# Kernel optimization log

Measured on AMD Instinct MI355X. Metric: run time of the kernel, lower is better.

The kernel has to match this reference:

```python
import jax, jax.numpy as jnp
import numpy as np
from jax import lax

B, IN_C, DIM, HEADS, K = 8, 64, 128, 4, 3
H, W = 96, 96
HEAD_DIM = DIM // HEADS
SCALE = HEAD_DIM ** -0.5
EPS = 1e-5  # BatchNorm eps (eval mode, running_mean=0, running_var=1)


def _conv3x3(x, w):
    return lax.conv_general_dilated(x, w, (1, 1), ((1, 1), (1, 1)),
                                    dimension_numbers=('NCHW', 'OIHW', 'NCHW'))


def _cbr(x, w, g, b):
    y = _conv3x3(x, w)
    y = y * (g / jnp.sqrt(1.0 + EPS))[None, :, None, None] + b[None, :, None, None]
    return jax.nn.relu(y)


def setup_inputs() -> dict:
    key = jax.random.key(0)
    ks = jax.random.split(key, 24)
    n = lambda i, s, sc=0.05: jax.random.normal(ks[i], s, jnp.float32) * sc
    u = lambda i, s: jax.random.uniform(ks[i], s, jnp.float32, 0.5, 1.5)
    return dict(
        x=jax.random.normal(ks[0], (B, IN_C, H, W), jnp.float32),
        fg=jax.random.normal(ks[1], (B, DIM, H, W), jnp.float32),
        conv1_w=n(2, (DIM, IN_C, 3, 3)), bn1_g=u(3, (DIM,)), bn1_b=n(4, (DIM,)),
        conv2_w=n(5, (DIM, DIM, 3, 3)), bn2_g=u(6, (DIM,)), bn2_b=n(7, (DIM,)),
        v_w=n(8, (DIM, DIM)), v_b=n(9, (DIM,)),
        attn_w=n(10, (K ** 4 * HEADS, DIM)), attn_b=n(11, (K ** 4 * HEADS,)),
        proj_w=n(12, (DIM, DIM)), proj_b=n(13, (DIM,)),
        conv3_w=n(14, (DIM, DIM, 3, 3)), bn3_g=u(15, (DIM,)), bn3_b=n(16, (DIM,)),
        conv4_w=n(17, (DIM, DIM, 3, 3)), bn4_g=u(18, (DIM,)), bn4_b=n(19, (DIM,)),
    )


def reference(x, fg, conv1_w, bn1_g, bn1_b, conv2_w, bn2_g, bn2_b,
              v_w, v_b, attn_w, attn_b, proj_w, proj_b,
              conv3_w, bn3_g, bn3_b, conv4_w, bn4_g, bn4_b):
    L = H * W
    # input_cbr: two conv3x3 + BN(eval) + ReLU
    xf = _cbr(_cbr(x, conv1_w, bn1_g, bn1_b), conv2_w, bn2_g, bn2_b)  # (B,DIM,H,W)
    xh = xf.transpose(0, 2, 3, 1)                 # (B,H,W,DIM)
    fgh = fg.transpose(0, 2, 3, 1)                # (B,H,W,DIM)
    # value projection then unfold (im2col, channel-major patch ordering like torch)
    v = (xh @ v_w.T + v_b).transpose(0, 3, 1, 2)  # (B,DIM,H,W)
    patches = lax.conv_general_dilated_patches(v, (K, K), (1, 1), ((1, 1), (1, 1)))  # (B,DIM*9,H,W)
    vp = patches.reshape(B, HEADS, HEAD_DIM, K * K, L).transpose(0, 1, 4, 3, 2)  # (B,h,L,9,hd)
    # attention logits directly from fg (stride=1 -> AvgPool identity)
    attn = (fgh @ attn_w.T + attn_b).reshape(B, L, HEADS, K * K, K * K)
    attn = attn.transpose(0, 2, 1, 3, 4) * SCALE  # (B,h,L,9,9)
    attn = jax.nn.softmax(attn, axis=-1)
    # batched small matmuls: (9,9) @ (9,hd) per window
    xw = jnp.einsum('bhlpq,bhlqd->bhlpd', attn, vp)  # (B,h,L,9,hd)
    xw = xw.transpose(0, 1, 4, 3, 2).reshape(B, DIM, K, K, H, W)  # channel-major, then (kh,kw)
    # fold: overlapping scatter-add back to (H,W)
    canvas = jnp.zeros((B, DIM, H + 2, W + 2), xw.dtype)
    for ki in range(K):
        for kj in range(K):
            canvas = canvas.at[:, :, ki:ki + H, kj:kj + W].add(xw[:, :, ki, kj])
    folded = canvas[:, :, 1:H + 1, 1:W + 1]        # crop padding
    p = (folded.transpose(0, 2, 3, 1) @ proj_w.T + proj_b).transpose(0, 3, 1, 2)
    # output_cbr
    out = _cbr(_cbr(p, conv3_w, bn3_g, bn3_b), conv4_w, bn4_g, bn4_b)
    return out
```

## Files before the change

kernel.cpp:

```cpp
#include <hip/hip_runtime.h>
#include <math.h>

typedef __attribute__((ext_vector_type(8))) short short8;
typedef __attribute__((ext_vector_type(4))) float f32x4;
typedef unsigned short u16;
typedef unsigned int u32;

#define HW   96
#define LPIX 9216
static constexpr float kScale = 0.17677669529663687f;

__device__ inline u16 f2bf(float f) {
    u32 x = __float_as_uint(f);
    return (u16)((x + 0x7fffu + ((x >> 16) & 1u)) >> 16);
}
__device__ inline float bf2f(u16 v) { return __uint_as_float((u32)v << 16); }

template <int C>
__global__ __launch_bounds__(256) void cast_nchw_nhwc(
    const float* __restrict__ in, u16* __restrict__ out)
{
    const int y = blockIdx.x, b = blockIdx.y, tid = threadIdx.x;
    __shared__ float sT[HW * C];
    for (int i = tid; i < HW * C; i += 256) {
        int c = i / HW, xx = i - c * HW;
        sT[xx * C + c] = in[(((size_t)b * C + c) * HW + y) * HW + xx];
    }
    __syncthreads();
    for (int i = tid; i < HW * (C / 8); i += 256) {
        int c8 = i % (C / 8), xx = i / (C / 8);
        union { short8 v8; u16 u[8]; } pk;
#pragma unroll
        for (int j = 0; j < 8; ++j) pk.u[j] = f2bf(sT[xx * C + c8 * 8 + j]);
        *(short8*)&out[(((size_t)b * HW + y) * HW + xx) * C + c8 * 8] = pk.v8;
    }
}

__global__ void cast_conv_w(const float* __restrict__ w, u16* __restrict__ wp, int CIN)
{
    int n = 9 * CIN * 128;
    int i = blockIdx.x * 256 + threadIdx.x;
    if (i >= n) return;
    int cil = i & 31; int t = i >> 5; int co = t & 127; int t2 = t >> 7;
    int nc5 = CIN >> 5;
    int c5 = t2 % nc5; int f = t2 / nc5;
    int ci = c5 * 32 + cil;
    wp[i] = f2bf(w[(size_t)(co * CIN + ci) * 9 + f]);
}

__global__ void cast_mat(const float* __restrict__ in, u16* __restrict__ out, int n)
{
    int i = blockIdx.x * 256 + threadIdx.x;
    if (i < n) out[i] = f2bf(in[i]);
}

template <int CIN, bool OUT_F32>
__global__ __launch_bounds__(256, 3) void conv_gemm(
    const u16* __restrict__ in, const u16* __restrict__ wp,
    const float* __restrict__ g, const float* __restrict__ be, void* outv)
{
    constexpr int NC6 = CIN / 64;
    constexpr int NC5 = CIN / 32;
    const int l0 = blockIdx.x * 128;
    const int b  = blockIdx.y;
    const int tid = threadIdx.x, lane = tid & 63, wv = tid >> 6;
    const int wm = wv >> 1, wn = wv & 1;
    const int lx = lane & 15, q = lane >> 4;

    __shared__ __align__(16) char smem[324 * 72 * 2];
    u16* sH = (u16*)smem;
    float* sT = (float*)smem;

    int py_[4], px_[4];
#pragma unroll
    for (int nt = 0; nt < 4; ++nt) {
        int l = l0 + wn * 64 + nt * 16 + lx;
        py_[nt] = l / 96; px_[nt] = l - py_[nt] * 96;
    }

    f32x4 acc[4][4];
#pragma unroll
    for (int mt = 0; mt < 4; ++mt)
#pragma unroll
        for (int nt = 0; nt < 4; ++nt) acc[mt][nt] = (f32x4){0.f, 0.f, 0.f, 0.f};

    for (int c6 = 0; c6 < NC6; ++c6) {
        __syncthreads();
        for (int t = tid; t < 2592; t += 256) {
            int k = t & 7, hp = t >> 3;
            int lh = l0 - 97 + hp;
            short8 v = {0, 0, 0, 0, 0, 0, 0, 0};
            if (lh >= 0 && lh < LPIX)
                v = *(const short8*)&in[((size_t)b * LPIX + lh) * CIN + c6 * 64 + k * 8];
            *(short8*)&sH[hp * 72 + k * 8] = v;
        }
        __syncthreads();

#pragma unroll
        for (int f = 0; f < 9; ++f) {
            const int dy = f / 3 - 1, dx = f % 3 - 1;
            const int off = dy * 96 + dx + 97;
            bool ok[4];
#pragma unroll
            for (int nt = 0; nt < 4; ++nt) {
                int yy = py_[nt] + dy, xx = px_[nt] + dx;
                ok[nt] = ((unsigned)yy < 96u) & ((unsigned)xx < 96u);
            }
#pragma unroll
            for (int kk = 0; kk < 2; ++kk) {
                short8 af[4], bfr[4];
#pragma unroll
                for (int mt = 0; mt < 4; ++mt)
                    af[mt] = *(const short8*)&wp[(size_t)(((f * NC5 + c6 * 2 + kk) * 128
                                                           + wm * 64 + mt * 16 + lx) * 32 + q * 8)];
#pragma unroll
                for (int nt = 0; nt < 4; ++nt) {
                    short8 t8 = *(const short8*)&sH[(wn * 64 + nt * 16 + lx + off) * 72
                                                    + kk * 32 + q * 8];
                    bfr[nt] = ok[nt] ? t8 : (short8){0, 0, 0, 0, 0, 0, 0, 0};
                }
#pragma unroll
                for (int mt = 0; mt < 4; ++mt)
#pragma unroll
                    for (int nt = 0; nt < 4; ++nt)
                        acc[mt][nt] = __builtin_amdgcn_mfma_f32_16x16x32_bf16(
                            af[mt], bfr[nt], acc[mt][nt], 0, 0, 0);
            }
        }
    }

    const float rs = rsqrtf(1.f + 1e-5f);
    if (OUT_F32) {
        float* out = (float*)outv;
#pragma unroll
        for (int mt = 0; mt < 4; ++mt) {
#pragma unroll
            for (int reg = 0; reg < 4; ++reg) {
                int co = wm * 64 + mt * 16 + q * 4 + reg;
                float sc = g[co] * rs, bb = be[co];
#pragma unroll
                for (int nt = 0; nt < 4; ++nt) {
                    int l = l0 + wn * 64 + nt * 16 + lx;
                    out[((size_t)b * 128 + co) * LPIX + l] =
                        fmaxf(fmaf(acc[mt][nt][reg], sc, bb), 0.f);
                }
            }
        }
    } else {
        u16* out = (u16*)outv;
        for (int mh = 0; mh < 2; ++mh) {
            __syncthreads();
            if (wm == mh) {
#pragma unroll
                for (int mt = 0; mt < 4; ++mt)
#pragma unroll
                    for (int nt = 0; nt < 4; ++nt)
#pragma unroll
                        for (int reg = 0; reg < 4; ++reg)
                            sT[(wn * 64 + nt * 16 + lx) * 65 + mt * 16 + q * 4 + reg] =
                                acc[mt][nt][reg];
            }
            __syncthreads();
            for (int i = tid; i < 1024; i += 256) {
                int cog = i & 7, px = i >> 3;
                union { short8 v8; u16 u[8]; } pk;
#pragma unroll
                for (int j = 0; j < 8; ++j) {
                    int co = mh * 64 + cog * 8 + j;
                    pk.u[j] = f2bf(fmaxf(fmaf(sT[px * 65 + cog * 8 + j], g[co] * rs, be[co]), 0.f));
                }
                *(short8*)&out[((size_t)b * LPIX + l0 + px) * 128 + mh * 64 + cog * 8] = pk.v8;
            }
        }
    }
}

__global__ __launch_bounds__(256) void linear_mfma(
    const u16* __restrict__ in, const u16* __restrict__ wp,
    const float* __restrict__ bias, u16* __restrict__ out)
{
    const int l0 = blockIdx.x * 64;
    const int tid = threadIdx.x, lane = tid & 63, wv = tid >> 6;
    const int wm = wv >> 1, wn = wv & 1;
    const int lx = lane & 15, q = lane >> 4;

    __shared__ char smem[4 * 64 * 40 * 2 + 4 * 128 * 40 * 2];
    u16* sX = (u16*)smem;
    u16* sW = (u16*)(smem + 4 * 64 * 40 * 2);
    float* sT = (float*)smem;

    for (int i = tid; i < 1024; i += 256) {
        int k8 = i & 15, px = i >> 4;
        short8 v = *(const short8*)&in[((size_t)(l0 + px)) * 128 + k8 * 8];
        *(short8*)&sX[((k8 >> 2) * 64 + px) * 40 + (k8 & 3) * 8] = v;
    }
    for (int i = tid; i < 2048; i += 256) {
        int k8 = i & 15, co = i >> 4;
        short8 v = *(const short8*)&wp[(size_t)co * 128 + k8 * 8];
        *(short8*)&sW[((k8 >> 2) * 128 + co) * 40 + (k8 & 3) * 8] = v;
    }
    __syncthreads();

    f32x4 acc[4][2];
#pragma unroll
    for (int mt = 0; mt < 4; ++mt)
#pragma unroll
        for (int nt = 0; nt < 2; ++nt) acc[mt][nt] = (f32x4){0.f, 0.f, 0.f, 0.f};

#pragma unroll
    for (int c4 = 0; c4 < 4; ++c4) {
        short8 af[4], bfr[2];
#pragma unroll
        for (int mt = 0; mt < 4; ++mt)
            af[mt] = *(const short8*)&sW[(c4 * 128 + wm * 64 + mt * 16 + lx) * 40 + q * 8];
#pragma unroll
        for (int nt = 0; nt < 2; ++nt)
            bfr[nt] = *(const short8*)&sX[(c4 * 64 + wn * 32 + nt * 16 + lx) * 40 + q * 8];
#pragma unroll
        for (int mt = 0; mt < 4; ++mt)
#pragma unroll
            for (int nt = 0; nt < 2; ++nt)
                acc[mt][nt] = __builtin_amdgcn_mfma_f32_16x16x32_bf16(
                    af[mt], bfr[nt], acc[mt][nt], 0, 0, 0);
    }

    for (int mh = 0; mh < 2; ++mh) {
        __syncthreads();
        if (wm == mh) {
#pragma unroll
            for (int mt = 0; mt < 4; ++mt)
#pragma unroll
                for (int nt = 0; nt < 2; ++nt)
#pragma unroll
                    for (int reg = 0; reg < 4; ++reg)
                        sT[(wn * 32 + nt * 16 + lx) * 65 + mt * 16 + q * 4 + reg] =
                            acc[mt][nt][reg];
        }
        __syncthreads();
        for (int i = tid; i < 512; i += 256) {
            int cog = i & 7, px = i >> 3;
            union { short8 v8; u16 u[8]; } pk;
#pragma unroll
            for (int j = 0; j < 8; ++j) {
                int co = mh * 64 + cog * 8 + j;
                pk.u[j] = f2bf(sT[px * 65 + cog * 8 + j] + bias[co]);
            }
            *(short8*)&out[((size_t)(l0 + px)) * 128 + mh * 64 + cog * 8] = pk.v8;
        }
    }
}

__global__ __launch_bounds__(256) void attn_mfma(
    const u16* __restrict__ fgb, const u16* __restrict__ awb,
    const float* __restrict__ ab, u16* __restrict__ A)
{
    const int lt = blockIdx.x, h = blockIdx.y, b = blockIdx.z;
    const int l0 = lt * 64;
    const int tid = threadIdx.x, lane = tid & 63, wv = tid >> 6;
    const int lx = lane & 15, q = lane >> 4;

    __shared__ char smem[4 * 64 * 40 * 2 + 4 * 96 * 40 * 2];
    u16* sX = (u16*)smem;
    u16* sW = (u16*)(smem + 4 * 64 * 40 * 2);
    float* sL = (float*)smem;

    for (int i = tid; i < 1024; i += 256) {
        int k8 = i & 15, px = i >> 4;
        short8 v = *(const short8*)&fgb[((size_t)b * LPIX + l0 + px) * 128 + k8 * 8];
        *(short8*)&sX[((k8 >> 2) * 64 + px) * 40 + (k8 & 3) * 8] = v;
    }
    for (int i = tid; i < 1536; i += 256) {
        int k8 = i & 15, rr = i >> 4;
        short8 v = {0, 0, 0, 0, 0, 0, 0, 0};
        if (rr < 81)
            v = *(const short8*)&awb[(size_t)(h * 81 + rr) * 128 + k8 * 8];
        *(short8*)&sW[((k8 >> 2) * 96 + rr) * 40 + (k8 & 3) * 8] = v;
    }
    __syncthreads();

    f32x4 acc[6];
#pragma unroll
    for (int j = 0; j < 6; ++j) acc[j] = (f32x4){0.f, 0.f, 0.f, 0.f};

#pragma unroll
    for (int c4 = 0; c4 < 4; ++c4) {
        short8 af = *(const short8*)&sX[(c4 * 64 + wv * 16 + lx) * 40 + q * 8];
#pragma unroll
        for (int j = 0; j < 6; ++j) {
            short8 bfr = *(const short8*)&sW[(c4 * 96 + j * 16 + lx) * 40 + q * 8];
            acc[j] = __builtin_amdgcn_mfma_f32_16x16x32_bf16(af, bfr, acc[j], 0, 0, 0);
        }
    }

    __syncthreads();
#pragma unroll
    for (int j = 0; j < 6; ++j)
#pragma unroll
        for (int reg = 0; reg < 4; ++reg)
            sL[(wv * 16 + q * 4 + reg) * 97 + j * 16 + lx] = acc[j][reg];
    __syncthreads();

    for (int t = tid; t < 576; t += 256) {
        int px = t & 63, p = t >> 6;
        const int rbase = h * 81 + p * 9;
        float lg[9], m = -1e30f;
#pragma unroll
        for (int qq = 0; qq < 9; ++qq) {
            lg[qq] = (sL[px * 97 + p * 9 + qq] + ab[rbase + qq]) * kScale;
            m = fmaxf(m, lg[qq]);
        }
        float s = 0.f;
#pragma unroll
        for (int qq = 0; qq < 9; ++qq) { lg[qq] = __expf(lg[qq] - m); s += lg[qq]; }
        float inv = 1.f / s;
        u16* Ab = &A[(((size_t)(b * 4 + h) * 9 + p) * 9) * LPIX + l0 + px];
#pragma unroll
        for (int qq = 0; qq < 9; ++qq) Ab[(size_t)qq * LPIX] = f2bf(lg[qq] * inv);
    }
}

__global__ __launch_bounds__(384, 4) void attn_fold(
    const u16* __restrict__ A, const u16* __restrict__ v,
    u16* __restrict__ out)
{
    const int yt = blockIdx.x, h = blockIdx.y, b = blockIdx.z;
    const int y0 = yt * 4;
    const int tid = threadIdx.x;
    const int yl  = tid / 96;
    const int x   = tid - yl * 96;
    const int y   = y0 + yl;
    const int l   = y * 96 + x;

    __shared__ u16 sV[8 * 96 * 32];

    const u16* vb = v + (size_t)b * LPIX * 128 + h * 32;
    for (int t = tid; t < 3072; t += 384) {
        int k = t & 3, s = t >> 2;
        int r = s / 96, xx = s - r * 96;
        int gy = y0 - 2 + r;
        uint4 uu = make_uint4(0u, 0u, 0u, 0u);
        if ((unsigned)gy < 96u)
            uu = *(const uint4*)&vb[(size_t)(gy * 96 + xx) * 128 + k * 8];
        *(uint4*)&sV[(size_t)s * 32 + k * 8] = uu;
    }

    float S[25];
#pragma unroll
    for (int i = 0; i < 25; ++i) S[i] = 0.f;

    const u16* Ab = A + ((size_t)(b * 4 + h) * 81) * (size_t)LPIX;
#pragma unroll
    for (int ki = 0; ki < 3; ++ki) {
        const int ly = y + 1 - ki;
        const bool vy = ((unsigned)ly < 96u);
#pragma unroll
        for (int kj = 0; kj < 3; ++kj) {
            const int lx2 = x + 1 - kj;
            if (vy && (unsigned)lx2 < 96u) {
                const u16* Ap = Ab + (size_t)(ki * 3 + kj) * 9 * (size_t)LPIX
                              + (ly * 96 + lx2);
#pragma unroll
                for (int qq = 0; qq < 9; ++qq) {
                    const int qi = qq / 3, qj = qq - qi * 3;
                    S[(qi - ki + 2) * 5 + (qj - kj + 2)] += bf2f(Ap[(size_t)qq * LPIX]);
                }
            }
        }
    }

    __syncthreads();

    float acc[32];
#pragma unroll
    for (int c = 0; c < 32; ++c) acc[c] = 0.f;

#pragma unroll
    for (int oy = 0; oy < 5; ++oy) {
        const int r = yl + oy;
#pragma unroll
        for (int ox = 0; ox < 5; ++ox) {
            const int xx = x + ox - 2;
            if ((unsigned)xx >= 96u) continue;
            const float sc = S[oy * 5 + ox];
            const u16* vp = &sV[(size_t)(r * 96 + xx) * 32];
#pragma unroll
            for (int c8 = 0; c8 < 4; ++c8) {
                const uint4 uu = *(const uint4*)&vp[c8 * 8];
                acc[c8 * 8 + 0] = fmaf(sc, __uint_as_float(uu.x << 16),          acc[c8 * 8 + 0]);
                acc[c8 * 8 + 1] = fmaf(sc, __uint_as_float(uu.x & 0xffff0000u), acc[c8 * 8 + 1]);
                acc[c8 * 8 + 2] = fmaf(sc, __uint_as_float(uu.y << 16),          acc[c8 * 8 + 2]);
                acc[c8 * 8 + 3] = fmaf(sc, __uint_as_float(uu.y & 0xffff0000u), acc[c8 * 8 + 3]);
                acc[c8 * 8 + 4] = fmaf(sc, __uint_as_float(uu.z << 16),          acc[c8 * 8 + 4]);
                acc[c8 * 8 + 5] = fmaf(sc, __uint_as_float(uu.z & 0xffff0000u), acc[c8 * 8 + 5]);
                acc[c8 * 8 + 6] = fmaf(sc, __uint_as_float(uu.w << 16),          acc[c8 * 8 + 6]);
                acc[c8 * 8 + 7] = fmaf(sc, __uint_as_float(uu.w & 0xffff0000u), acc[c8 * 8 + 7]);
            }
        }
    }

    u16* ob = &out[((size_t)b * LPIX + l) * 128 + h * 32];
#pragma unroll
    for (int gidx = 0; gidx < 4; ++gidx) {
        union { short8 v8; u16 u[8]; } pk;
#pragma unroll
        for (int j = 0; j < 8; ++j) pk.u[j] = f2bf(acc[gidx * 8 + j]);
        *(short8*)&ob[gidx * 8] = pk.v8;
    }
}

extern "C" void kernel_launch(void* const* d_in, const int* in_sizes, int n_in,
                              void* d_out, int out_size, void* d_ws, size_t ws_size,
                              hipStream_t stream)
{
    const float* x    = (const float*)d_in[0];
    const float* fg   = (const float*)d_in[1];
    const float* c1w  = (const float*)d_in[2];
    const float* bn1g = (const float*)d_in[3];
    const float* bn1b = (const float*)d_in[4];
    const float* c2w  = (const float*)d_in[5];
    const float* bn2g = (const float*)d_in[6];
    const float* bn2b = (const float*)d_in[7];
    const float* vw   = (const float*)d_in[8];
    const float* vb   = (const float*)d_in[9];
    const float* aw   = (const float*)d_in[10];
    const float* abv  = (const float*)d_in[11];
    const float* pw   = (const float*)d_in[12];
    const float* pb   = (const float*)d_in[13];
    const float* c3w  = (const float*)d_in[14];
    const float* bn3g = (const float*)d_in[15];
    const float* bn3b = (const float*)d_in[16];
    const float* c4w  = (const float*)d_in[17];
    const float* bn4g = (const float*)d_in[18];
    const float* bn4b = (const float*)d_in[19];

    char* wsp = (char*)d_ws;
    size_t off = 0;
    auto carve = [&](size_t bytes) {
        void* pp = wsp + off;
        off += (bytes + 255) & ~(size_t)255;
        return pp;
    };
    u16*   xb   = (u16*)carve((size_t)8 * LPIX * 64 * 2);
    u16*   fgb  = (u16*)carve((size_t)8 * LPIX * 128 * 2);
    u16*   actA = (u16*)carve((size_t)8 * LPIX * 128 * 2);
    u16*   actB = (u16*)carve((size_t)8 * LPIX * 128 * 2);
    u16*   Abuf = (u16*)carve((size_t)8 * 324 * LPIX * 2);
    u16*   w1p  = (u16*)carve((size_t)9 * 2 * 128 * 32 * 2);
    u16*   w2p  = (u16*)carve((size_t)9 * 4 * 128 * 32 * 2);
    u16*   w3p  = (u16*)carve((size_t)9 * 4 * 128 * 32 * 2);
    u16*   w4p  = (u16*)carve((size_t)9 * 4 * 128 * 32 * 2);
    u16*   vwp  = (u16*)carve((size_t)128 * 128 * 2);
    u16*   pwp  = (u16*)carve((size_t)128 * 128 * 2);
    u16*   awb  = (u16*)carve((size_t)324 * 128 * 2);

    cast_nchw_nhwc<64><<<dim3(HW, 8), 256, 0, stream>>>(x, xb);
    cast_nchw_nhwc<128><<<dim3(HW, 8), 256, 0, stream>>>(fg, fgb);
    cast_conv_w<<<(9 * 64 * 128 + 255) / 256, 256, 0, stream>>>(c1w, w1p, 64);
    cast_conv_w<<<(9 * 128 * 128 + 255) / 256, 256, 0, stream>>>(c2w, w2p, 128);
    cast_conv_w<<<(9 * 128 * 128 + 255) / 256, 256, 0, stream>>>(c3w, w3p, 128);
    cast_conv_w<<<(9 * 128 * 128 + 255) / 256, 256, 0, stream>>>(c4w, w4p, 128);
    cast_mat<<<(16384 + 255) / 256, 256, 0, stream>>>(vw, vwp, 16384);
    cast_mat<<<(16384 + 255) / 256, 256, 0, stream>>>(pw, pwp, 16384);
    cast_mat<<<(324 * 128 + 255) / 256, 256, 0, stream>>>(aw, awb, 324 * 128);

    conv_gemm<64, false><<<dim3(72, 8), 256, 0, stream>>>(xb, w1p, bn1g, bn1b, actA);
    conv_gemm<128, false><<<dim3(72, 8), 256, 0, stream>>>(actA, w2p, bn2g, bn2b, actB);
    linear_mfma<<<1152, 256, 0, stream>>>(actB, vwp, vb, actA);
    attn_mfma<<<dim3(144, 4, 8), 256, 0, stream>>>(fgb, awb, abv, Abuf);
    attn_fold<<<dim3(24, 4, 8), 384, 0, stream>>>(Abuf, actA, actB);
    linear_mfma<<<1152, 256, 0, stream>>>(actB, pwp, pb, actA);
    conv_gemm<128, false><<<dim3(72, 8), 256, 0, stream>>>(actA, w3p, bn3g, bn3b, actB);
    conv_gemm<128, true><<<dim3(72, 8), 256, 0, stream>>>(actB, w4p, bn4g, bn4b, d_out);
}
```

Before: 411.5 us.

## Double-buffer conv halo loads in 32-channel chunks with 96-pixel tiles

Restructures the implicit-GEMM conv kernel to stage the input halo in 32-channel chunks across two LDS buffers. The next chunk is prefetched into registers while the current one is computed, replacing the load-sync-compute pattern over 64-channel chunks. The pixel tile shrinks from 128 to 96 (one image row), so the grid grows from 72 to 96 blocks per batch. This aims to hide global load latency and improve CU fill, at the cost of more barriers and less reuse of weight fragments per block.

Result: no change. 418.6 us (+1.7%).

```diff
diff --git a/kernel.cpp b/kernel.cpp
--- a/kernel.cpp
+++ b/kernel.cpp
@@ -59,75 +59,111 @@
     const u16* __restrict__ in, const u16* __restrict__ wp,
     const float* __restrict__ g, const float* __restrict__ be, void* outv)
 {
-    constexpr int NC6 = CIN / 64;
-    constexpr int NC5 = CIN / 32;
-    const int l0 = blockIdx.x * 128;
+    constexpr int NC     = CIN / 32;
+    constexpr int HROWS  = 290;
+    constexpr int HPITCH = 40;
+    constexpr int NGRAN  = HROWS * 4;
+
+    const int l0 = blockIdx.x * 96;
     const int b  = blockIdx.y;
     const int tid = threadIdx.x, lane = tid & 63, wv = tid >> 6;
     const int wm = wv >> 1, wn = wv & 1;
     const int lx = lane & 15, q = lane >> 4;
 
-    __shared__ __align__(16) char smem[324 * 72 * 2];
-    u16* sH = (u16*)smem;
+    __shared__ __align__(16) char smem[2 * HROWS * HPITCH * 2];
     float* sT = (float*)smem;
 
-    int py_[4], px_[4];
-#pragma unroll
-    for (int nt = 0; nt < 4; ++nt) {
-        int l = l0 + wn * 64 + nt * 16 + lx;
+    int py_[3], px_[3];
+#pragma unroll
+    for (int nt = 0; nt < 3; ++nt) {
+        int l = l0 + wn * 48 + nt * 16 + lx;
         py_[nt] = l / 96; px_[nt] = l - py_[nt] * 96;
     }
 
-    f32x4 acc[4][4];
+    f32x4 acc[4][3];
 #pragma unroll
     for (int mt = 0; mt < 4; ++mt)
 #pragma unroll
-        for (int nt = 0; nt < 4; ++nt) acc[mt][nt] = (f32x4){0.f, 0.f, 0.f, 0.f};
-
-    for (int c6 = 0; c6 < NC6; ++c6) {
-        __syncthreads();
-        for (int t = tid; t < 2592; t += 256) {
-            int k = t & 7, hp = t >> 3;
-            int lh = l0 - 97 + hp;
-            short8 v = {0, 0, 0, 0, 0, 0, 0, 0};
-            if (lh >= 0 && lh < LPIX)
-                v = *(const short8*)&in[((size_t)b * LPIX + lh) * CIN + c6 * 64 + k * 8];
-            *(short8*)&sH[hp * 72 + k * 8] = v;
-        }
-        __syncthreads();
-
+        for (int nt = 0; nt < 3; ++nt) acc[mt][nt] = (f32x4){0.f, 0.f, 0.f, 0.f};
+
+    const u16* inb = in + (size_t)b * LPIX * CIN;
+    short8 st[5];
+
+    auto LOADC = [&](int c) {
+#pragma unroll
+        for (int i = 0; i < 5; ++i) {
+            int gi = tid + i * 256;
+            short8 v = (short8){0, 0, 0, 0, 0, 0, 0, 0};
+            if (gi < NGRAN) {
+                int hp = gi >> 2, k = gi & 3;
+                int lh = l0 - 97 + hp;
+                if ((unsigned)lh < (unsigned)LPIX)
+                    v = *(const short8*)&inb[(size_t)lh * CIN + c * 32 + k * 8];
+            }
+            st[i] = v;
+        }
+    };
+    auto WRITEC = [&](int bsel) {
+        u16* sB = (u16*)smem + bsel * (HROWS * HPITCH);
+#pragma unroll
+        for (int i = 0; i < 5; ++i) {
+            int gi = tid + i * 256;
+            if (gi < NGRAN)
+                *(short8*)&sB[(gi >> 2) * HPITCH + (gi & 3) * 8] = st[i];
+        }
+    };
+    auto COMPUTE = [&](int c, int bsel) {
+        const u16* sB = (const u16*)smem + bsel * (HROWS * HPITCH);
 #pragma unroll
         for (int f = 0; f < 9; ++f) {
             const int dy = f / 3 - 1, dx = f % 3 - 1;
             const int off = dy * 96 + dx + 97;
-            bool ok[4];
-#pragma unroll
-            for (int nt = 0; nt < 4; ++nt) {
+            bool ok[3];
+#pragma unroll
+            for (int nt = 0; nt < 3; ++nt) {
                 int yy = py_[nt] + dy, xx = px_[nt] + dx;
                 ok[nt] = ((unsigned)yy < 96u) & ((unsigned)xx < 96u);
             }
-#pragma unroll
-            for (int kk = 0; kk < 2; ++kk) {
-                short8 af[4], bfr[4];
-#pragma unroll
-                for (int mt = 0; mt < 4; ++mt)
-                    af[mt] = *(const short8*)&wp[(size_t)(((f * NC5 + c6 * 2 + kk) * 128
-                                                           + wm * 64 + mt * 16 + lx) * 32 + q * 8)];
-#pragma unroll
-                for (int nt = 0; nt < 4; ++nt) {
-                    short8 t8 = *(const short8*)&sH[(wn * 64 + nt * 16 + lx + off) * 72
-                                                    + kk * 32 + q * 8];
-                    bfr[nt] = ok[nt] ? t8 : (short8){0, 0, 0, 0, 0, 0, 0, 0};
-                }
-#pragma unroll
-                for (int mt = 0; mt < 4; ++mt)
-#pragma unroll
-                    for (int nt = 0; nt < 4; ++nt)
-                        acc[mt][nt] = __builtin_amdgcn_mfma_f32_16x16x32_bf16(
-                            af[mt], bfr[nt], acc[mt][nt], 0, 0, 0);
-            }
-        }
-    }
+            short8 af[4], bfr[3];
+#pragma unroll
+            for (int mt = 0; mt < 4; ++mt)
+                af[mt] = *(const short8*)&wp[(size_t)(((f * NC + c) * 128
+                                                       + wm * 64 + mt * 16 + lx) * 32 + q * 8)];
+#pragma unroll
+            for (int nt = 0; nt < 3; ++nt) {
+                short8 t8 = *(const short8*)&sB[(wn * 48 + nt * 16 + lx + off) * HPITCH + q * 8];
+                bfr[nt] = ok[nt] ? t8 : (short8){0, 0, 0, 0, 0, 0, 0, 0};
+            }
+#pragma unroll
+            for (int mt = 0; mt < 4; ++mt)
+#pragma unroll
+                for (int nt = 0; nt < 3; ++nt)
+                    acc[mt][nt] = __builtin_amdgcn_mfma_f32_16x16x32_bf16(
+                        af[mt], bfr[nt], acc[mt][nt], 0, 0, 0);
+        }
+    };
+
+#define CHUNK_BAR() do {                                             \
+        asm volatile("s_waitcnt lgkmcnt(0)" ::: "memory");           \
+        __builtin_amdgcn_s_barrier();                                \
+        asm volatile("" ::: "memory");                               \
+    } while (0)
+
+    LOADC(0);
+    WRITEC(0);
+    LOADC(1);
+    CHUNK_BAR();
+
+#pragma unroll
+    for (int c = 0; c < NC; ++c) {
+        COMPUTE(c, c & 1);
+        if (c + 1 < NC) {
+            WRITEC((c + 1) & 1);
+            if (c + 2 < NC) LOADC(c + 2);
+            CHUNK_BAR();
+        }
+    }
+#undef CHUNK_BAR
 
     const float rs = rsqrtf(1.f + 1e-5f);
     if (OUT_F32) {
@@ -139,8 +175,8 @@
                 int co = wm * 64 + mt * 16 + q * 4 + reg;
                 float sc = g[co] * rs, bb = be[co];
 #pragma unroll
-                for (int nt = 0; nt < 4; ++nt) {
-                    int l = l0 + wn * 64 + nt * 16 + lx;
+                for (int nt = 0; nt < 3; ++nt) {
+                    int l = l0 + wn * 48 + nt * 16 + lx;
                     out[((size_t)b * 128 + co) * LPIX + l] =
                         fmaxf(fmaf(acc[mt][nt][reg], sc, bb), 0.f);
                 }
@@ -154,14 +190,14 @@
 #pragma unroll
                 for (int mt = 0; mt < 4; ++mt)
 #pragma unroll
-                    for (int nt = 0; nt < 4; ++nt)
+                    for (int nt = 0; nt < 3; ++nt)
 #pragma unroll
                         for (int reg = 0; reg < 4; ++reg)
-                            sT[(wn * 64 + nt * 16 + lx) * 65 + mt * 16 + q * 4 + reg] =
+                            sT[(wn * 48 + nt * 16 + lx) * 65 + mt * 16 + q * 4 + reg] =
                                 acc[mt][nt][reg];
             }
             __syncthreads();
-            for (int i = tid; i < 1024; i += 256) {
+            for (int i = tid; i < 768; i += 256) {
                 int cog = i & 7, px = i >> 3;
                 union { short8 v8; u16 u[8]; } pk;
 #pragma unroll
@@ -463,12 +499,12 @@
     cast_mat<<<(16384 + 255) / 256, 256, 0, stream>>>(pw, pwp, 16384);
     cast_mat<<<(324 * 128 + 255) / 256, 256, 0, stream>>>(aw, awb, 324 * 128);
 
-    conv_gemm<64, false><<<dim3(72, 8), 256, 0, stream>>>(xb, w1p, bn1g, bn1b, actA);
-    conv_gemm<128, false><<<dim3(72, 8), 256, 0, stream>>>(actA, w2p, bn2g, bn2b, actB);
+    conv_gemm<64, false><<<dim3(96, 8), 256, 0, stream>>>(xb, w1p, bn1g, bn1b, actA);
+    conv_gemm<128, false><<<dim3(96, 8), 256, 0, stream>>>(actA, w2p, bn2g, bn2b, actB);
     linear_mfma<<<1152, 256, 0, stream>>>(actB, vwp, vb, actA);
     attn_mfma<<<dim3(144, 4, 8), 256, 0, stream>>>(fgb, awb, abv, Abuf);
     attn_fold<<<dim3(24, 4, 8), 384, 0, stream>>>(Abuf, actA, actB);
     linear_mfma<<<1152, 256, 0, stream>>>(actB, pwp, pb, actA);
-    conv_gemm<128, false><<<dim3(72, 8), 256, 0, stream>>>(actA, w3p, bn3g, bn3b, actB);
-    conv_gemm<128, true><<<dim3(72, 8), 256, 0, stream>>>(actB, w4p, bn4g, bn4b, d_out);
-}
+    conv_gemm<128, false><<<dim3(96, 8), 256, 0, stream>>>(actA, w3p, bn3g, bn3b, actB);
+    conv_gemm<128, true><<<dim3(96, 8), 256, 0, stream>>>(actB, w4p, bn4g, bn4b, d_out);
+}
```

## Restructure conv GEMM tiles with direct global-to-LDS loads and swizzled layouts

Applied to the files above, without the earlier changes.

Reworks the 3x3 conv implicit GEMM so each block computes 64 output channels over three image rows, using three waves per block. Weights are staged into LDS alongside the input halo instead of being read from global memory per MFMA. Staging uses global_load_lds with an XOR-style swizzled layout, and the weight packing kernel is changed to match. The aim is to cut redundant global weight traffic and LDS bank conflicts, and to simplify boundary masking. In exchange it uses more LDS per block, which lowers occupancy, and the loads are not double-buffered.

Result: faster. 368.2 us (-10.5%).

```diff
diff --git a/kernel.cpp b/kernel.cpp
--- a/kernel.cpp
+++ b/kernel.cpp
@@ -15,6 +15,12 @@
     return (u16)((x + 0x7fffu + ((x >> 16) & 1u)) >> 16);
 }
 __device__ inline float bf2f(u16 v) { return __uint_as_float((u32)v << 16); }
+
+typedef __attribute__((address_space(1))) const void gas_t;
+typedef __attribute__((address_space(3))) void las_t;
+__device__ __forceinline__ void g2lds16(const void* g, void* l) {
+    __builtin_amdgcn_global_load_lds((gas_t*)g, (las_t*)l, 16, 0, 0);
+}
 
 template <int C>
 __global__ __launch_bounds__(256) void cast_nchw_nhwc(
@@ -41,10 +47,18 @@
     int n = 9 * CIN * 128;
     int i = blockIdx.x * 256 + threadIdx.x;
     if (i >= n) return;
-    int cil = i & 31; int t = i >> 5; int co = t & 127; int t2 = t >> 7;
-    int nc5 = CIN >> 5;
-    int c5 = t2 % nc5; int f = t2 / nc5;
-    int ci = c5 * 32 + cil;
+    int NC = CIN >> 5;
+    int e  = i & 7;
+    int gr = i >> 3;
+    int cc = gr / 2304;
+    int gi = gr - cc * 2304;
+    int coh = cc / NC, c = cc - coh * NC;
+    int f = gi >> 8;
+    int m = (gi >> 2) & 63;
+    int s = gi & 3;
+    int qq = (s - (m >> 1)) & 3;
+    int co = coh * 64 + m;
+    int ci = c * 32 + qq * 8 + e;
     wp[i] = f2bf(w[(size_t)(co * CIN + ci) * 9 + f]);
 }
 
@@ -55,77 +69,91 @@
 }
 
 template <int CIN, bool OUT_F32>
-__global__ __launch_bounds__(256, 3) void conv_gemm(
+__global__ __launch_bounds__(192, 2) void conv_gemm(
     const u16* __restrict__ in, const u16* __restrict__ wp,
     const float* __restrict__ g, const float* __restrict__ be, void* outv)
 {
-    constexpr int NC6 = CIN / 64;
-    constexpr int NC5 = CIN / 32;
-    const int l0 = blockIdx.x * 128;
-    const int b  = blockIdx.y;
+    constexpr int NC    = CIN / 32;
+    constexpr int WBYT  = 36864;
+    constexpr int NHG   = 1928;
+
+    const int bx  = blockIdx.x;
+    const int b   = blockIdx.y;
+    const int coh = bx >> 5;
+    const int gg  = bx & 31;
+    const int gsw = (gg & 7) * 4 + (gg >> 3);
+    const int y0  = gsw * 3;
+    const int l0h = y0 * 96 - 97;
+
     const int tid = threadIdx.x, lane = tid & 63, wv = tid >> 6;
-    const int wm = wv >> 1, wn = wv & 1;
     const int lx = lane & 15, q = lane >> 4;
 
-    __shared__ __align__(16) char smem[324 * 72 * 2];
-    u16* sH = (u16*)smem;
+    __shared__ __align__(16) char smem[WBYT + NHG * 16];
     float* sT = (float*)smem;
 
-    int py_[4], px_[4];
-#pragma unroll
-    for (int nt = 0; nt < 4; ++nt) {
-        int l = l0 + wn * 64 + nt * 16 + lx;
-        py_[nt] = l / 96; px_[nt] = l - py_[nt] * 96;
-    }
-
-    f32x4 acc[4][4];
+    const int aoff = lx * 64 + (((q + (lx >> 1)) & 3) << 4);
+    const int pb   = wv * 96 + lx;
+
+    f32x4 acc[4][6];
 #pragma unroll
     for (int mt = 0; mt < 4; ++mt)
 #pragma unroll
-        for (int nt = 0; nt < 4; ++nt) acc[mt][nt] = (f32x4){0.f, 0.f, 0.f, 0.f};
-
-    for (int c6 = 0; c6 < NC6; ++c6) {
-        __syncthreads();
-        for (int t = tid; t < 2592; t += 256) {
-            int k = t & 7, hp = t >> 3;
-            int lh = l0 - 97 + hp;
-            short8 v = {0, 0, 0, 0, 0, 0, 0, 0};
-            if (lh >= 0 && lh < LPIX)
-                v = *(const short8*)&in[((size_t)b * LPIX + lh) * CIN + c6 * 64 + k * 8];
-            *(short8*)&sH[hp * 72 + k * 8] = v;
-        }
-        __syncthreads();
+        for (int nt = 0; nt < 6; ++nt) acc[mt][nt] = (f32x4){0.f, 0.f, 0.f, 0.f};
+
+    const u16* inb = in + (size_t)b * LPIX * CIN;
+
+#pragma unroll
+    for (int c = 0; c < NC; ++c) {
+        if (c) __syncthreads();
+
+        {
+            const u16* wqb = wp + ((size_t)(coh * NC + c)) * 2304 * 8;
+#pragma unroll
+            for (int j = 0; j < 12; ++j) {
+                int gj = j * 192 + tid;
+                g2lds16(&wqb[(size_t)gj * 8],
+                        (char*)smem + (j * 192 + wv * 64) * 16);
+            }
+        }
+#pragma unroll
+        for (int i = 0; i < 11; ++i) {
+            int gi = i * 192 + tid;
+            if (gi < NHG) {
+                int p = gi >> 2, s = gi & 3;
+                int qq = (s - (p >> 1)) & 3;
+                int lh = l0h + p;
+                lh = lh < 0 ? 0 : (lh >= LPIX ? LPIX - 1 : lh);
+                g2lds16(&inb[(size_t)lh * CIN + c * 32 + qq * 8],
+                        (char*)smem + WBYT + (i * 192 + wv * 64) * 16);
+            }
+        }
+        asm volatile("s_waitcnt vmcnt(0)" ::: "memory");
+        __builtin_amdgcn_s_barrier();
+        asm volatile("" ::: "memory");
 
 #pragma unroll
         for (int f = 0; f < 9; ++f) {
             const int dy = f / 3 - 1, dx = f % 3 - 1;
             const int off = dy * 96 + dx + 97;
-            bool ok[4];
-#pragma unroll
-            for (int nt = 0; nt < 4; ++nt) {
-                int yy = py_[nt] + dy, xx = px_[nt] + dx;
-                ok[nt] = ((unsigned)yy < 96u) & ((unsigned)xx < 96u);
-            }
-#pragma unroll
-            for (int kk = 0; kk < 2; ++kk) {
-                short8 af[4], bfr[4];
-#pragma unroll
-                for (int mt = 0; mt < 4; ++mt)
-                    af[mt] = *(const short8*)&wp[(size_t)(((f * NC5 + c6 * 2 + kk) * 128
-                                                           + wm * 64 + mt * 16 + lx) * 32 + q * 8)];
-#pragma unroll
-                for (int nt = 0; nt < 4; ++nt) {
-                    short8 t8 = *(const short8*)&sH[(wn * 64 + nt * 16 + lx + off) * 72
-                                                    + kk * 32 + q * 8];
-                    bfr[nt] = ok[nt] ? t8 : (short8){0, 0, 0, 0, 0, 0, 0, 0};
-                }
-#pragma unroll
-                for (int mt = 0; mt < 4; ++mt)
-#pragma unroll
-                    for (int nt = 0; nt < 4; ++nt)
-                        acc[mt][nt] = __builtin_amdgcn_mfma_f32_16x16x32_bf16(
-                            af[mt], bfr[nt], acc[mt][nt], 0, 0, 0);
-            }
+            const bool vy = (unsigned)(y0 + wv + dy) < 96u;
+            short8 af[4], bfr[6];
+#pragma unroll
+            for (int mt = 0; mt < 4; ++mt)
+                af[mt] = *(const short8*)((const char*)smem + f * 4096 + mt * 1024 + aoff);
+#pragma unroll
+            for (int nt = 0; nt < 6; ++nt) {
+                int p = pb + nt * 16 + off;
+                int slot = (q + (p >> 1)) & 3;
+                short8 t8 = *(const short8*)((const char*)smem + WBYT + p * 64 + slot * 16);
+                bool ok = vy & ((unsigned)(nt * 16 + lx + dx) < 96u);
+                bfr[nt] = ok ? t8 : (short8){0, 0, 0, 0, 0, 0, 0, 0};
+            }
+#pragma unroll
+            for (int mt = 0; mt < 4; ++mt)
+#pragma unroll
+                for (int nt = 0; nt < 6; ++nt)
+                    acc[mt][nt] = __builtin_amdgcn_mfma_f32_16x16x32_bf16(
+                        af[mt], bfr[nt], acc[mt][nt], 0, 0, 0);
         }
     }
 
@@ -136,11 +164,11 @@
         for (int mt = 0; mt < 4; ++mt) {
 #pragma unroll
             for (int reg = 0; reg < 4; ++reg) {
-                int co = wm * 64 + mt * 16 + q * 4 + reg;
+                int co = coh * 64 + mt * 16 + q * 4 + reg;
                 float sc = g[co] * rs, bb = be[co];
 #pragma unroll
-                for (int nt = 0; nt < 4; ++nt) {
-                    int l = l0 + wn * 64 + nt * 16 + lx;
+                for (int nt = 0; nt < 6; ++nt) {
+                    int l = (y0 + wv) * 96 + nt * 16 + lx;
                     out[((size_t)b * 128 + co) * LPIX + l] =
                         fmaxf(fmaf(acc[mt][nt][reg], sc, bb), 0.f);
                 }
@@ -148,28 +176,31 @@
         }
     } else {
         u16* out = (u16*)outv;
-        for (int mh = 0; mh < 2; ++mh) {
+#pragma unroll
+        for (int hh = 0; hh < 2; ++hh) {
             __syncthreads();
-            if (wm == mh) {
-#pragma unroll
-                for (int mt = 0; mt < 4; ++mt)
-#pragma unroll
-                    for (int nt = 0; nt < 4; ++nt)
-#pragma unroll
-                        for (int reg = 0; reg < 4; ++reg)
-                            sT[(wn * 64 + nt * 16 + lx) * 65 + mt * 16 + q * 4 + reg] =
-                                acc[mt][nt][reg];
-            }
+#pragma unroll
+            for (int mt = 0; mt < 4; ++mt)
+#pragma unroll
+                for (int nn = 0; nn < 3; ++nn) {
+                    int nt = hh * 3 + nn;
+#pragma unroll
+                    for (int reg = 0; reg < 4; ++reg)
+                        sT[(wv * 48 + nn * 16 + lx) * 65 + mt * 16 + q * 4 + reg] =
+                            acc[mt][nt][reg];
+                }
             __syncthreads();
-            for (int i = tid; i < 1024; i += 256) {
-                int cog = i & 7, px = i >> 3;
+            for (int i = tid; i < 1152; i += 192) {
+                int cog = i & 7, pxl = i >> 3;
+                int wrr = pxl / 48, ofs = pxl - wrr * 48;
+                int l = (y0 + wrr) * 96 + hh * 48 + ofs;
                 union { short8 v8; u16 u[8]; } pk;
 #pragma unroll
                 for (int j = 0; j < 8; ++j) {
-                    int co = mh * 64 + cog * 8 + j;
-                    pk.u[j] = f2bf(fmaxf(fmaf(sT[px * 65 + cog * 8 + j], g[co] * rs, be[co]), 0.f));
+                    int co = coh * 64 + cog * 8 + j;
+                    pk.u[j] = f2bf(fmaxf(fmaf(sT[pxl * 65 + cog * 8 + j], g[co] * rs, be[co]), 0.f));
                 }
-                *(short8*)&out[((size_t)b * LPIX + l0 + px) * 128 + mh * 64 + cog * 8] = pk.v8;
+                *(short8*)&out[((size_t)b * LPIX + l) * 128 + coh * 64 + cog * 8] = pk.v8;
             }
         }
     }
@@ -463,12 +494,12 @@
     cast_mat<<<(16384 + 255) / 256, 256, 0, stream>>>(pw, pwp, 16384);
     cast_mat<<<(324 * 128 + 255) / 256, 256, 0, stream>>>(aw, awb, 324 * 128);
 
-    conv_gemm<64, false><<<dim3(72, 8), 256, 0, stream>>>(xb, w1p, bn1g, bn1b, actA);
-    conv_gemm<128, false><<<dim3(72, 8), 256, 0, stream>>>(actA, w2p, bn2g, bn2b, actB);
+    conv_gemm<64, false><<<dim3(64, 8), 192, 0, stream>>>(xb, w1p, bn1g, bn1b, actA);
+    conv_gemm<128, false><<<dim3(64, 8), 192, 0, stream>>>(actA, w2p, bn2g, bn2b, actB);
     linear_mfma<<<1152, 256, 0, stream>>>(actB, vwp, vb, actA);
     attn_mfma<<<dim3(144, 4, 8), 256, 0, stream>>>(fgb, awb, abv, Abuf);
     attn_fold<<<dim3(24, 4, 8), 384, 0, stream>>>(Abuf, actA, actB);
     linear_mfma<<<1152, 256, 0, stream>>>(actB, pwp, pb, actA);
-    conv_gemm<128, false><<<dim3(72, 8), 256, 0, stream>>>(actA, w3p, bn3g, bn3b, actB);
-    conv_gemm<128, true><<<dim3(72, 8), 256, 0, stream>>>(actB, w4p, bn4g, bn4b, d_out);
-}
+    conv_gemm<128, false><<<dim3(64, 8), 192, 0, stream>>>(actA, w3p, bn3g, bn3b, actB);
+    conv_gemm<128, true><<<dim3(64, 8), 192, 0, stream>>>(actB, w4p, bn4g, bn4b, d_out);
+}
```
